# Kernel optimization log

Measured on AMD Instinct MI355X. Metric: run time of the kernel, lower is better.

Reference implementation:

```python
import jax, jax.numpy as jnp
import numpy as np

EMB = 1024
HEADS = 16
BLOCK = 128


def setup_inputs() -> dict:
    key = jax.random.key(0)
    k1, k2, k3 = jax.random.split(key, 3)
    B, T, C = 4, 4096, EMB
    x = jax.random.normal(k1, (B, T, C), dtype=jnp.float32)
    # Linear weights stored as [in, out] (i.e. torch W.T); qkv has no bias.
    W_qkv = jax.random.normal(k2, (C, 3 * C), dtype=jnp.float32) * 0.02
    W_proj = jax.random.normal(k3, (C, C), dtype=jnp.float32) * 0.02
    b_proj = jnp.zeros((C,), dtype=jnp.float32)
    return {"x": x, "W_qkv": W_qkv, "W_proj": W_proj, "b_proj": b_proj}


def reference(x, W_qkv, W_proj, b_proj):
    # Dropout is inference-mode identity.
    B, T, C = x.shape
    H, D, BS = HEADS, C // HEADS, BLOCK
    nb = T // BS  # number of local blocks
    qkv = x @ W_qkv  # [B,T,3C]
    q, k, v = jnp.split(qkv, 3, axis=-1)
    # [B, nb, BS, H, D] -- each block attends only within itself
    q = q.reshape(B, nb, BS, H, D)
    k = k.reshape(B, nb, BS, H, D)
    v = v.reshape(B, nb, BS, H, D)
    scores = jnp.einsum("bnqhd,bnkhd->bnhqk", q, k) / jnp.sqrt(jnp.float32(D))
    # is_decoder: causal tril within each diagonal block (tril[i:end, i:end])
    tril = jnp.tril(jnp.ones((BS, BS), dtype=bool))
    scores = jnp.where(tril, scores, -jnp.inf)
    # faithful to original: stable exp, then divide by (sum + 1e-6)
    scores = scores - jnp.max(scores, axis=-1, keepdims=True)
    e = jnp.exp(scores)
    p = e / (jnp.sum(e, axis=-1, keepdims=True) + 1e-6)
    out = jnp.einsum("bnhqk,bnkhd->bnqhd", p, v).reshape(B, T, C)
    return out @ W_proj + b_proj
```

## Files before the change

### kernel.cpp

```cpp
#include <hip/hip_runtime.h>
#include <hip/hip_bf16.h>
#include <math.h>


typedef __bf16 bf16_t;
typedef __bf16 bf16x8 __attribute__((ext_vector_type(8)));
typedef float  f32x4  __attribute__((ext_vector_type(4)));

typedef const __attribute__((address_space(1))) void* gptr_t;
typedef __attribute__((address_space(3))) void* lptr_t;

__global__ __launch_bounds__(256) void cvt_f32_bf16(const float* __restrict__ in,
                                                    bf16_t* __restrict__ out, size_t n) {
    size_t stride = (size_t)gridDim.x * blockDim.x * 4;
    for (size_t i = ((size_t)blockIdx.x * blockDim.x + threadIdx.x) * 4; i < n; i += stride) {
        float4 v = *(const float4*)(in + i);
        bf16_t t[4];
        t[0] = (bf16_t)v.x; t[1] = (bf16_t)v.y; t[2] = (bf16_t)v.z; t[3] = (bf16_t)v.w;
        *(uint2*)(out + i) = *(uint2*)t;
    }
}

__global__ __launch_bounds__(256) void transpose_cvt(const float* __restrict__ in,
                                                     bf16_t* __restrict__ out, int K, int N) {
    __shared__ float tile[32][33];
    const int tx = threadIdx.x & 31, ty = threadIdx.x >> 5;
    const int bx = blockIdx.x, by = blockIdx.y;
    #pragma unroll
    for (int i = 0; i < 4; i++) {
        const int k = by * 32 + ty + i * 8;
        tile[ty + i * 8][tx] = in[(size_t)k * N + bx * 32 + tx];
    }
    __syncthreads();
    #pragma unroll
    for (int i = 0; i < 4; i++) {
        const int n = bx * 32 + ty + i * 8;
        out[(size_t)n * K + by * 32 + tx] = (bf16_t)tile[tx][ty + i * 8];
    }
}

template <bool BF16_OUT, bool BIAS>
__global__ __launch_bounds__(512, 2) void gemm256(const bf16_t* __restrict__ A,
                                                  const bf16_t* __restrict__ Bt,
                                                  void* __restrict__ Cout,
                                                  const float* __restrict__ bias,
                                                  int M, int N, int K) {
    __shared__ bf16_t As[4][256 * 32];
    __shared__ bf16_t Bs[4][256 * 32];

    const int tid  = threadIdx.x;
    const int lane = tid & 63, wave = tid >> 6;
    const int quad = lane >> 4, l16 = lane & 15;
    const int wm = wave >> 2, wn = wave & 3;

    const int nbm  = M >> 8;
    const int mloc = nbm >> 3;
    const int xcd  = blockIdx.x & 7;
    const int idx  = blockIdx.x >> 3;
    const int bn   = idx / mloc;
    const int bm   = xcd * mloc + (idx - bn * mloc);

    const bf16_t* Ab = A  + (size_t)bm * 256 * K;
    const bf16_t* Bb = Bt + (size_t)bn * 256 * K;

    const int srow = lane >> 2;
    const int scs  = (lane & 3) ^ ((srow >> 1) & 3);
    const int rdo  = ((quad ^ ((l16 >> 1) & 3)) << 3);

    f32x4 acc[8][4];
    #pragma unroll
    for (int i = 0; i < 8; ++i)
        #pragma unroll
        for (int j = 0; j < 4; ++j) acc[i][j] = (f32x4){0.f, 0.f, 0.f, 0.f};

#define STG(ARR, SRC, SLICE, I)                                                       \
    __builtin_amdgcn_global_load_lds(                                                 \
        (gptr_t)((SRC) + (size_t)(wave * 32 + (I) * 16 + srow) * K + ((SLICE) << 5) + \
                 scs * 8),                                                            \
        (lptr_t)&(ARR)[(SLICE) & 3][(wave * 32 + (I) * 16) * 32], 16, 0, 0)

#define SLICE_BODY(KS, DO_STAGE, WAIT_STMT)                                           \
    do {                                                                              \
        const int ks_ = (KS);                                                         \
        const bf16_t* Asl_ = As[ks_ & 3];                                             \
        const bf16_t* Bsl_ = Bs[ks_ & 3];                                             \
        bf16x8 af_[8], bf_[4];                                                        \
                             \
        _Pragma("unroll")                                                             \
        for (int fr = 0; fr < 4; ++fr)                                                \
            af_[fr] = *(const bf16x8*)&Asl_[(wm * 128 + fr * 16 + l16) * 32 + rdo];   \
        _Pragma("unroll")                                                             \
        for (int fr = 0; fr < 4; ++fr)                                                \
            bf_[fr] = *(const bf16x8*)&Bsl_[(wn * 64 + fr * 16 + l16) * 32 + rdo];    \
        if (DO_STAGE) { STG(As, Ab, ks_ + 3, 0); STG(As, Ab, ks_ + 3, 1); }           \
        __builtin_amdgcn_s_barrier();                                                 \
        asm volatile("s_waitcnt lgkmcnt(0)" ::: "memory");                            \
        __builtin_amdgcn_s_setprio(1);                                                \
        _Pragma("unroll")                                                             \
        for (int mr = 0; mr < 4; ++mr)                                                \
            _Pragma("unroll")                                                         \
            for (int nr = 0; nr < 4; ++nr)                                            \
                acc[mr][nr] = __builtin_amdgcn_mfma_f32_16x16x32_bf16(                \
                    af_[mr], bf_[nr], acc[mr][nr], 0, 0, 0);                          \
        __builtin_amdgcn_s_setprio(0);                                                \
        __builtin_amdgcn_s_barrier();                                                 \
              \
        _Pragma("unroll")                                                             \
        for (int fr = 0; fr < 4; ++fr)                                                \
            af_[4 + fr] =                                                             \
                *(const bf16x8*)&Asl_[(wm * 128 + (4 + fr) * 16 + l16) * 32 + rdo];   \
        if (DO_STAGE) { STG(Bs, Bb, ks_ + 3, 0); STG(Bs, Bb, ks_ + 3, 1); }           \
        WAIT_STMT;                                                                    \
        __builtin_amdgcn_s_barrier();                                                 \
        asm volatile("s_waitcnt lgkmcnt(0)" ::: "memory");                            \
        __builtin_amdgcn_s_setprio(1);                                                \
        _Pragma("unroll")                                                             \
        for (int mr = 0; mr < 4; ++mr)                                                \
            _Pragma("unroll")                                                         \
            for (int nr = 0; nr < 4; ++nr)                                            \
                acc[4 + mr][nr] = __builtin_amdgcn_mfma_f32_16x16x32_bf16(            \
                    af_[4 + mr], bf_[nr], acc[4 + mr][nr], 0, 0, 0);                  \
        __builtin_amdgcn_s_setprio(0);                                                \
        __builtin_amdgcn_s_barrier();                                                 \
    } while (0)

    STG(As, Ab, 0, 0); STG(As, Ab, 0, 1); STG(Bs, Bb, 0, 0); STG(Bs, Bb, 0, 1);
    STG(As, Ab, 1, 0); STG(As, Ab, 1, 1); STG(Bs, Bb, 1, 0); STG(Bs, Bb, 1, 1);
    STG(As, Ab, 2, 0); STG(As, Ab, 2, 1); STG(Bs, Bb, 2, 0); STG(Bs, Bb, 2, 1);
    asm volatile("s_waitcnt vmcnt(8)" ::: "memory");
    __builtin_amdgcn_s_barrier();

    const int NS = K >> 5;
    for (int ks = 0; ks < NS - 3; ++ks)
        SLICE_BODY(ks, true, asm volatile("s_waitcnt vmcnt(8)" ::: "memory"));
    SLICE_BODY(NS - 3, false, asm volatile("s_waitcnt vmcnt(4)" ::: "memory"));
    SLICE_BODY(NS - 2, false, asm volatile("s_waitcnt vmcnt(0)" ::: "memory"));
    SLICE_BODY(NS - 1, false, (void)0);
#undef SLICE_BODY
#undef STG

    #pragma unroll
    for (int mr = 0; mr < 8; ++mr) {
        #pragma unroll
        for (int nr = 0; nr < 4; ++nr) {
            const int gcol = bn * 256 + wn * 64 + nr * 16 + l16;
            #pragma unroll
            for (int reg = 0; reg < 4; ++reg) {
                const int grow = bm * 256 + wm * 128 + mr * 16 + quad * 4 + reg;
                float v = acc[mr][nr][reg];
                if (BIAS) v += bias[gcol];
                if (BF16_OUT)
                    ((bf16_t*)Cout)[(size_t)grow * N + gcol] = (bf16_t)v;
                else
                    ((float*)Cout)[(size_t)grow * N + gcol] = v;
            }
        }
    }
}

__global__ __launch_bounds__(256, 3) void attn_kernel(const bf16_t* __restrict__ qkv,
                                                      bf16_t* __restrict__ attn_out) {
    __shared__ __align__(16) char smem[54272];
    bf16_t* qs = (bf16_t*)smem;
    bf16_t* ks = (bf16_t*)(smem + 18432);
    bf16_t* vT = (bf16_t*)(smem + 36864);
    bf16_t* ps = (bf16_t*)smem;

    const int tid = threadIdx.x;
    const int lane = tid & 63, wave = tid >> 6;
    const int quad = lane >> 4, l16 = lane & 15;

    const int bid = blockIdx.x;
    const int h = bid & 15;
    const int blk = (bid >> 4) & 31;
    const int b = bid >> 9;
    const int row0 = (b * 32 + blk) * 128;
    const int LDQ = 3072;

    for (int t = tid; t < 128 * 8; t += 256) {
        const int r = t >> 3;
        const int c = (t & 7) * 8;
        const bf16_t* src = qkv + (size_t)(row0 + r) * LDQ + h * 64;
        *(uint4*)&qs[r * 72 + c] = *(const uint4*)(src + c);
        *(uint4*)&ks[r * 72 + c] = *(const uint4*)(src + 1024 + c);
        bf16x8 vv = *(const bf16x8*)(src + 2048 + c);
        #pragma unroll
        for (int j = 0; j < 8; j++)
            vT[(c + j) * 136 + r] = vv[j];
    }
    __syncthreads();

    f32x4 sfrag[2][8];
    for (int mr = 0; mr < 2; mr++)
        for (int nc = 0; nc < 8; nc++)
            sfrag[mr][nc] = (f32x4){0.f, 0.f, 0.f, 0.f};

    #pragma unroll
    for (int ksl = 0; ksl < 2; ksl++) {
        bf16x8 aq[2], bk[8];
        #pragma unroll
        for (int mr = 0; mr < 2; mr++)
            aq[mr] = *(const bf16x8*)&qs[(wave * 32 + mr * 16 + l16) * 72 + ksl * 32 + quad * 8];
        #pragma unroll
        for (int nc = 0; nc < 8; nc++)
            bk[nc] = *(const bf16x8*)&ks[(nc * 16 + l16) * 72 + ksl * 32 + quad * 8];
        #pragma unroll
        for (int mr = 0; mr < 2; mr++)
            #pragma unroll
            for (int nc = 0; nc < 8; nc++)
                sfrag[mr][nc] = __builtin_amdgcn_mfma_f32_16x16x32_bf16(aq[mr], bk[nc], sfrag[mr][nc], 0, 0, 0);
    }

    #pragma unroll
    for (int mr = 0; mr < 2; mr++) {
        #pragma unroll
        for (int nc = 0; nc < 8; nc++) {
            #pragma unroll
            for (int reg = 0; reg < 4; reg++) {
                const int row = wave * 32 + mr * 16 + quad * 4 + reg;
                const int col = nc * 16 + l16;
                float s = sfrag[mr][nc][reg] * 0.125f;
                if (col > row) s = -INFINITY;
                sfrag[mr][nc][reg] = s;
            }
        }
    }

    #pragma unroll
    for (int mr = 0; mr < 2; mr++) {
        #pragma unroll
        for (int reg = 0; reg < 4; reg++) {
            float m = -INFINITY;
            #pragma unroll
            for (int nc = 0; nc < 8; nc++) m = fmaxf(m, sfrag[mr][nc][reg]);
            #pragma unroll
            for (int off = 1; off < 16; off <<= 1) m = fmaxf(m, __shfl_xor(m, off));
            float sum = 0.f;
            #pragma unroll
            for (int nc = 0; nc < 8; nc++) {
                float e = __expf(sfrag[mr][nc][reg] - m);
                sfrag[mr][nc][reg] = e;
                sum += e;
            }
            #pragma unroll
            for (int off = 1; off < 16; off <<= 1) sum += __shfl_xor(sum, off);
            const float inv = 1.0f / (sum + 1e-6f);
            #pragma unroll
            for (int nc = 0; nc < 8; nc++) sfrag[mr][nc][reg] *= inv;
        }
    }

    __syncthreads();

    #pragma unroll
    for (int mr = 0; mr < 2; mr++)
        #pragma unroll
        for (int nc = 0; nc < 8; nc++)
            #pragma unroll
            for (int reg = 0; reg < 4; reg++) {
                const int row = wave * 32 + mr * 16 + quad * 4 + reg;
                const int col = nc * 16 + l16;
                ps[row * 136 + col] = (bf16_t)sfrag[mr][nc][reg];
            }
    __syncthreads();

    f32x4 oacc[2][4];
    for (int mr = 0; mr < 2; mr++)
        for (int nd = 0; nd < 4; nd++)
            oacc[mr][nd] = (f32x4){0.f, 0.f, 0.f, 0.f};

    #pragma unroll
    for (int ksl = 0; ksl < 4; ksl++) {
        bf16x8 ap[2];
        #pragma unroll
        for (int mr = 0; mr < 2; mr++)
            ap[mr] = *(const bf16x8*)&ps[(wave * 32 + mr * 16 + l16) * 136 + ksl * 32 + quad * 8];
        #pragma unroll
        for (int nd = 0; nd < 4; nd++) {
            bf16x8 bv = *(const bf16x8*)&vT[(nd * 16 + l16) * 136 + ksl * 32 + quad * 8];
            #pragma unroll
            for (int mr = 0; mr < 2; mr++)
                oacc[mr][nd] = __builtin_amdgcn_mfma_f32_16x16x32_bf16(ap[mr], bv, oacc[mr][nd], 0, 0, 0);
        }
    }

    #pragma unroll
    for (int mr = 0; mr < 2; mr++)
        #pragma unroll
        for (int nd = 0; nd < 4; nd++)
            #pragma unroll
            for (int reg = 0; reg < 4; reg++) {
                const int row = row0 + wave * 32 + mr * 16 + quad * 4 + reg;
                const int col = h * 64 + nd * 16 + l16;
                attn_out[(size_t)row * 1024 + col] = (bf16_t)oacc[mr][nd][reg];
            }
}

extern "C" void kernel_launch(void* const* d_in, const int* in_sizes, int n_in,
                              void* d_out, int out_size, void* d_ws, size_t ws_size,
                              hipStream_t stream) {
    const float* x     = (const float*)d_in[0];
    const float* Wqkv  = (const float*)d_in[1];
    const float* Wproj = (const float*)d_in[2];
    const float* bproj = (const float*)d_in[3];

    const int M = 16384, C = 1024, N1 = 3072;

    char* ws = (char*)d_ws;
    bf16_t* xb     = (bf16_t*)(ws);
    bf16_t* wqkvT  = (bf16_t*)(ws + 33554432);
    bf16_t* wprojT = (bf16_t*)(ws + 39845888);
    bf16_t* qkvb   = (bf16_t*)(ws + 41943040);
    bf16_t* attnb  = (bf16_t*)(ws + 142606336);

    cvt_f32_bf16<<<8192, 256, 0, stream>>>(x, xb, (size_t)M * C);
    transpose_cvt<<<dim3(N1 / 32, C / 32), 256, 0, stream>>>(Wqkv, wqkvT, C, N1);
    transpose_cvt<<<dim3(C / 32, C / 32), 256, 0, stream>>>(Wproj, wprojT, C, C);

    gemm256<true, false><<<(N1 / 256) * (M / 256), 512, 0, stream>>>(
        xb, wqkvT, (void*)qkvb, nullptr, M, N1, C);

    attn_kernel<<<2048, 256, 0, stream>>>(qkvb, attnb);

    gemm256<false, true><<<(C / 256) * (M / 256), 512, 0, stream>>>(
        attnb, wprojT, d_out, bproj, M, C, C);
}
```

Before: 316.4 us.

## Shrink GEMM tile to 128x256 with a 3-slot unified LDS ring

```diff
diff --git a/kernel.cpp b/kernel.cpp
--- a/kernel.cpp
+++ b/kernel.cpp
@@ -40,61 +40,67 @@
 }
 
 template <bool BF16_OUT, bool BIAS>
-__global__ __launch_bounds__(512, 2) void gemm256(const bf16_t* __restrict__ A,
-                                                  const bf16_t* __restrict__ Bt,
-                                                  void* __restrict__ Cout,
-                                                  const float* __restrict__ bias,
-                                                  int M, int N, int K) {
-    __shared__ bf16_t As[4][256 * 32];
-    __shared__ bf16_t Bs[4][256 * 32];
+__global__ __launch_bounds__(512) void gemm128(const bf16_t* __restrict__ A,
+                                               const bf16_t* __restrict__ Bt,
+                                               void* __restrict__ Cout,
+                                               const float* __restrict__ bias,
+                                               int M, int N, int K) {
+    __shared__ bf16_t ring[3][12288];
 
     const int tid  = threadIdx.x;
     const int lane = tid & 63, wave = tid >> 6;
     const int quad = lane >> 4, l16 = lane & 15;
     const int wm = wave >> 2, wn = wave & 3;
 
-    const int nbm  = M >> 8;
+    const int nbm  = M >> 7;
     const int mloc = nbm >> 3;
     const int xcd  = blockIdx.x & 7;
     const int idx  = blockIdx.x >> 3;
     const int bn   = idx / mloc;
     const int bm   = xcd * mloc + (idx - bn * mloc);
 
-    const bf16_t* Ab = A  + (size_t)bm * 256 * K;
+    const bf16_t* Ab = A  + (size_t)bm * 128 * K;
     const bf16_t* Bb = Bt + (size_t)bn * 256 * K;
 
     const int srow = lane >> 2;
     const int scs  = (lane & 3) ^ ((srow >> 1) & 3);
     const int rdo  = ((quad ^ ((l16 >> 1) & 3)) << 3);
 
-    f32x4 acc[8][4];
-    #pragma unroll
-    for (int i = 0; i < 8; ++i)
+    f32x4 acc[4][4];
+    #pragma unroll
+    for (int i = 0; i < 4; ++i)
         #pragma unroll
         for (int j = 0; j < 4; ++j) acc[i][j] = (f32x4){0.f, 0.f, 0.f, 0.f};
 
-#define STG(ARR, SRC, SLICE, I)                                                       \
-    __builtin_amdgcn_global_load_lds(                                                 \
-        (gptr_t)((SRC) + (size_t)(wave * 32 + (I) * 16 + srow) * K + ((SLICE) << 5) + \
-                 scs * 8),                                                            \
-        (lptr_t)&(ARR)[(SLICE) & 3][(wave * 32 + (I) * 16) * 32], 16, 0, 0)
-
-#define SLICE_BODY(KS, DO_STAGE, WAIT_STMT)                                           \
+#define STG(SLICE, SLOT)                                                              \
     do {                                                                              \
-        const int ks_ = (KS);                                                         \
-        const bf16_t* Asl_ = As[ks_ & 3];                                             \
-        const bf16_t* Bsl_ = Bs[ks_ & 3];                                             \
-        bf16x8 af_[8], bf_[4];                                                        \
-                             \
+        __builtin_amdgcn_global_load_lds(                                             \
+            (gptr_t)(Ab + (size_t)(wave * 16 + srow) * K + ((SLICE) << 5) + scs * 8), \
+            (lptr_t)&ring[SLOT][wave * 512], 16, 0, 0);                               \
+        __builtin_amdgcn_global_load_lds(                                             \
+            (gptr_t)(Bb + (size_t)(wave * 32 + srow) * K + ((SLICE) << 5) + scs * 8), \
+            (lptr_t)&ring[SLOT][4096 + wave * 1024], 16, 0, 0);                       \
+        __builtin_amdgcn_global_load_lds(                                             \
+            (gptr_t)(Bb + (size_t)(wave * 32 + 16 + srow) * K + ((SLICE) << 5) +      \
+                     scs * 8),                                                        \
+            (lptr_t)&ring[SLOT][4096 + wave * 1024 + 512], 16, 0, 0);                 \
+    } while (0)
+
+#define BODY(G, RS, SS, DO_STAGE, WAIT_STMT)                                          \
+    do {                                                                              \
+        const bf16_t* sl_ = ring[RS];                                                 \
+        bf16x8 af_[4], bf_[4];                                                        \
         _Pragma("unroll")                                                             \
         for (int fr = 0; fr < 4; ++fr)                                                \
-            af_[fr] = *(const bf16x8*)&Asl_[(wm * 128 + fr * 16 + l16) * 32 + rdo];   \
+            af_[fr] = *(const bf16x8*)&sl_[(wm * 64 + fr * 16 + l16) * 32 + rdo];     \
         _Pragma("unroll")                                                             \
         for (int fr = 0; fr < 4; ++fr)                                                \
-            bf_[fr] = *(const bf16x8*)&Bsl_[(wn * 64 + fr * 16 + l16) * 32 + rdo];    \
-        if (DO_STAGE) { STG(As, Ab, ks_ + 3, 0); STG(As, Ab, ks_ + 3, 1); }           \
+            bf_[fr] =                                                                 \
+                *(const bf16x8*)&sl_[4096 + (wn * 64 + fr * 16 + l16) * 32 + rdo];    \
+        if (DO_STAGE) STG((G) + 2, SS);                                               \
+        asm volatile("s_waitcnt lgkmcnt(0)" ::: "memory");                            \
+        WAIT_STMT;                                                                    \
         __builtin_amdgcn_s_barrier();                                                 \
-        asm volatile("s_waitcnt lgkmcnt(0)" ::: "memory");                            \
         __builtin_amdgcn_s_setprio(1);                                                \
         _Pragma("unroll")                                                             \
         for (int mr = 0; mr < 4; ++mr)                                                \
@@ -103,50 +109,33 @@
                 acc[mr][nr] = __builtin_amdgcn_mfma_f32_16x16x32_bf16(                \
                     af_[mr], bf_[nr], acc[mr][nr], 0, 0, 0);                          \
         __builtin_amdgcn_s_setprio(0);                                                \
-        __builtin_amdgcn_s_barrier();                                                 \
-              \
-        _Pragma("unroll")                                                             \
-        for (int fr = 0; fr < 4; ++fr)                                                \
-            af_[4 + fr] =                                                             \
-                *(const bf16x8*)&Asl_[(wm * 128 + (4 + fr) * 16 + l16) * 32 + rdo];   \
-        if (DO_STAGE) { STG(Bs, Bb, ks_ + 3, 0); STG(Bs, Bb, ks_ + 3, 1); }           \
-        WAIT_STMT;                                                                    \
-        __builtin_amdgcn_s_barrier();                                                 \
-        asm volatile("s_waitcnt lgkmcnt(0)" ::: "memory");                            \
-        __builtin_amdgcn_s_setprio(1);                                                \
-        _Pragma("unroll")                                                             \
-        for (int mr = 0; mr < 4; ++mr)                                                \
-            _Pragma("unroll")                                                         \
-            for (int nr = 0; nr < 4; ++nr)                                            \
-                acc[4 + mr][nr] = __builtin_amdgcn_mfma_f32_16x16x32_bf16(            \
-                    af_[4 + mr], bf_[nr], acc[4 + mr][nr], 0, 0, 0);                  \
-        __builtin_amdgcn_s_setprio(0);                                                \
-        __builtin_amdgcn_s_barrier();                                                 \
     } while (0)
 
-    STG(As, Ab, 0, 0); STG(As, Ab, 0, 1); STG(Bs, Bb, 0, 0); STG(Bs, Bb, 0, 1);
-    STG(As, Ab, 1, 0); STG(As, Ab, 1, 1); STG(Bs, Bb, 1, 0); STG(Bs, Bb, 1, 1);
-    STG(As, Ab, 2, 0); STG(As, Ab, 2, 1); STG(Bs, Bb, 2, 0); STG(Bs, Bb, 2, 1);
-    asm volatile("s_waitcnt vmcnt(8)" ::: "memory");
+    STG(0, 0); STG(1, 1);
+    asm volatile("s_waitcnt vmcnt(3)" ::: "memory");
     __builtin_amdgcn_s_barrier();
 
     const int NS = K >> 5;
-    for (int ks = 0; ks < NS - 3; ++ks)
-        SLICE_BODY(ks, true, asm volatile("s_waitcnt vmcnt(8)" ::: "memory"));
-    SLICE_BODY(NS - 3, false, asm volatile("s_waitcnt vmcnt(4)" ::: "memory"));
-    SLICE_BODY(NS - 2, false, asm volatile("s_waitcnt vmcnt(0)" ::: "memory"));
-    SLICE_BODY(NS - 1, false, (void)0);
-#undef SLICE_BODY
+    int rs = 0, ss = 2;
+    for (int g = 0; g < NS - 2; ++g) {
+        BODY(g, rs, ss, true, asm volatile("s_waitcnt vmcnt(3)" ::: "memory"));
+        rs = (rs == 2) ? 0 : rs + 1;
+        ss = (ss == 2) ? 0 : ss + 1;
+    }
+    BODY(NS - 2, rs, ss, false, asm volatile("s_waitcnt vmcnt(0)" ::: "memory"));
+    rs = (rs == 2) ? 0 : rs + 1;
+    BODY(NS - 1, rs, ss, false, (void)0);
+#undef BODY
 #undef STG
 
     #pragma unroll
-    for (int mr = 0; mr < 8; ++mr) {
+    for (int mr = 0; mr < 4; ++mr) {
         #pragma unroll
         for (int nr = 0; nr < 4; ++nr) {
             const int gcol = bn * 256 + wn * 64 + nr * 16 + l16;
             #pragma unroll
             for (int reg = 0; reg < 4; ++reg) {
-                const int grow = bm * 256 + wm * 128 + mr * 16 + quad * 4 + reg;
+                const int grow = bm * 128 + wm * 64 + mr * 16 + quad * 4 + reg;
                 float v = acc[mr][nr][reg];
                 if (BIAS) v += bias[gcol];
                 if (BF16_OUT)
@@ -317,11 +306,11 @@
     transpose_cvt<<<dim3(N1 / 32, C / 32), 256, 0, stream>>>(Wqkv, wqkvT, C, N1);
     transpose_cvt<<<dim3(C / 32, C / 32), 256, 0, stream>>>(Wproj, wprojT, C, C);
 
-    gemm256<true, false><<<(N1 / 256) * (M / 256), 512, 0, stream>>>(
+    gemm128<true, false><<<(N1 / 256) * (M / 128), 512, 0, stream>>>(
         xb, wqkvT, (void*)qkvb, nullptr, M, N1, C);
 
     attn_kernel<<<2048, 256, 0, stream>>>(qkvb, attnb);
 
-    gemm256<false, true><<<(C / 256) * (M / 256), 512, 0, stream>>>(
+    gemm128<false, true><<<(C / 256) * (M / 128), 512, 0, stream>>>(
         attnb, wprojT, d_out, bproj, M, C, C);
 }
```

New measurement: 325.7 us. 2.9% more time.
